# Performance work log

Hardware: AMD Instinct MI355X
Metric: run time of the kernel (lower is better)

Reference implementation:

```python
import jax, jax.numpy as jnp
import numpy as np

IN_SIZE = 1024
HID = 2048
OUT = 1024
M_STEPS = 100   # max extra ponder steps -> up to M_STEPS+1 total steps
EPS = 0.01


def setup_inputs() -> dict:
    key = jax.random.key(0)
    ks = jax.random.split(key, 11)
    inv = 1.0 / np.sqrt(HID)

    def unif(k, shape, scale):
        return jax.random.uniform(k, shape, jnp.float32, -scale, scale)

    return {
        "x": jax.random.normal(ks[0], (IN_SIZE,), jnp.float32),
        "h0": jax.random.normal(ks[1], (HID,), jnp.float32) * 0.1,
        "c0": jax.random.normal(ks[2], (HID,), jnp.float32) * 0.1,
        "W_ih": unif(ks[3], (4 * HID, 1 + IN_SIZE), inv),
        "b_ih": unif(ks[4], (4 * HID,), inv),
        "W_hh": unif(ks[5], (4 * HID, HID), inv),
        "b_hh": unif(ks[6], (4 * HID,), inv),
        "w_halt": unif(ks[7], (HID,), inv),
        "b_halt": jnp.ones((1,), jnp.float32),  # fc_halt.bias = 1.0 per source
        "W_out": unif(ks[8], (OUT, HID), inv),
        "b_out": unif(ks[9], (OUT,), inv),
    }


def reference(x, h0, c0, W_ih, b_ih, W_hh, b_hh, w_halt, b_halt, W_out, b_out):
    # Input contribution is constant across steps except the prepended halt flag
    # (1 on first step, 0 after). Precompute it once.
    ih_x = W_ih[:, 1:] @ x + b_ih + b_hh      # (4H,)
    w_flag = W_ih[:, 0]                        # (4H,)

    def step(carry, flag):
        h, c = carry
        gates = ih_x + flag * w_flag + W_hh @ h  # (4H,)
        i, f, g, o = jnp.split(gates, 4)
        i = jax.nn.sigmoid(i)
        f = jax.nn.sigmoid(f)
        g = jnp.tanh(g)
        o = jax.nn.sigmoid(o)
        c = f * c + i * g
        h = o * jnp.tanh(c)
        return (h, c), (h, c)

    flags = jnp.concatenate(
        [jnp.ones((1,), x.dtype), jnp.zeros((M_STEPS,), x.dtype)])
    _, (H, C) = jax.lax.scan(step, (h0, c0), flags)  # (M+1, HID) each

    p = jax.nn.sigmoid(H @ w_halt + b_halt[0])       # (M+1,) halting probs
    csum = jnp.cumsum(p)
    halted = csum >= 1.0 - EPS
    # n = first step where cumulative halt prob crosses threshold, capped at M
    n = jnp.where(jnp.any(halted), jnp.argmax(halted), M_STEPS)
    # remainder r = 1 - sum(p[:n]); csum[n] - p[n] == sum(p[:n])
    r = 1.0 - jnp.where(n > 0, csum[n] - p[n], 0.0)

    idx = jnp.arange(M_STEPS + 1)
    w = jnp.where(idx < n, p, jnp.where(idx == n, r, 0.0))  # (M+1,)

    outputs = H @ W_out.T + b_out                    # (M+1, OUT)
    output = w @ outputs                             # (OUT,) weights sum to 1
    h_out = w @ H                                    # (HID,)
    c_out = w @ C                                    # (HID,)
    ponder = n.astype(x.dtype) + 1.0 + r
    return output, (h_out, c_out), ponder
```

## Files before the change

### kernel.cpp

```cpp
#include <hip/hip_runtime.h>


#define HID    2048
#define INS    1024
#define OUTS   1024
#define MSTEPS 100
#define NBLK   256
#define NTHR   512
#define NWAVE  8
#define JPB    8
#define RPB    32
#define SLOTF  16

typedef unsigned long long u64;
typedef unsigned int u32;

__device__ __forceinline__ float wave_allreduce(float v) {
    #pragma unroll
    for (int off = 32; off > 0; off >>= 1)
        v += __shfl_xor(v, off, 64);
    return v;
}

__device__ __forceinline__ u64 aload(const u64* p) {
    return __hip_atomic_load(p, __ATOMIC_RELAXED, __HIP_MEMORY_SCOPE_AGENT);
}
__device__ __forceinline__ void astore(u64* p, u64 v) {
    __hip_atomic_store(p, v, __ATOMIC_RELAXED, __HIP_MEMORY_SCOPE_AGENT);
}
__device__ __forceinline__ void astoref(float* p, float v) {
    __hip_atomic_store(p, v, __ATOMIC_RELAXED, __HIP_MEMORY_SCOPE_AGENT);
}


__global__
__attribute__((amdgpu_flat_work_group_size(NTHR, NTHR)))
__attribute__((amdgpu_waves_per_eu(2, 2)))
void alstm_kernel(
    const float* __restrict__ x,      const float* __restrict__ h0,
    const float* __restrict__ c0,     const float* __restrict__ W_ih,
    const float* __restrict__ b_ih,   const float* __restrict__ W_hh,
    const float* __restrict__ b_hh,   const float* __restrict__ w_halt,
    const float* __restrict__ b_halt, const float* __restrict__ W_out,
    const float* __restrict__ b_out,  float* __restrict__ out,
    float* __restrict__ ws)
{
    const int b    = blockIdx.x;
    const int tid  = threadIdx.x;
    const int wave = tid >> 6;
    const int lane = tid & 63;

    float* arrive = ws;
    float* hbuf0  = ws + NBLK * SLOTF;
    float* hbuf1  = hbuf0 + HID;

    __shared__ float x_lds[INS];
    __shared__ float hjoint[HID];
    __shared__ float hcur[HID];
    __shared__ float gate_lds[RPB];
    __shared__ float ihx_lds[RPB];
    __shared__ float psum[NWAVE];

    const int j_own = b * JPB + tid;
    const int lr0   = 4 * wave;
    const int rbase = (lr0 >> 3) * HID + b * JPB + (lr0 & 7);

    #define DOT4(H4P, G0, G1, G2, G3) do {                                     \
        const float4* h4__ = (H4P);                                            \
        _Pragma("unroll")                                                      \
        for (int m = 0; m < 8; ++m) {                                          \
            float4 hh = h4__[lane + 64 * m];                                   \
            G0 += wa0[m].x*hh.x + wa0[m].y*hh.y + wa0[m].z*hh.z + wa0[m].w*hh.w; \
            G1 += wa1[m].x*hh.x + wa1[m].y*hh.y + wa1[m].z*hh.z + wa1[m].w*hh.w; \
            G2 += wa2[m].x*hh.x + wa2[m].y*hh.y + wa2[m].z*hh.z + wa2[m].w*hh.w; \
            G3 += wa3[m].x*hh.x + wa3[m].y*hh.y + wa3[m].z*hh.z + wa3[m].w*hh.w; \
        }                                                                      \
    } while (0)

    const float bh = b_halt[0];
    float2 xv  = ((const float2*)x)[tid];
    float4 h0v = ((const float4*)h0)[tid];
    float4 wh4 = ((const float4*)w_halt)[tid];
    float c_reg = (tid < JPB) ? c0[j_own] : 0.f;
    float bo    = (tid < 4)   ? b_out[b * 4 + tid] : 0.f;
    float bsum = 0.f, wflg = 0.f;
    if (lane < 4) {
        const int lr = lr0 + lane;
        const int r  = (lr >> 3) * HID + b * JPB + (lr & 7);
        bsum = b_ih[r] + b_hh[r];
        wflg = W_ih[(size_t)r * (INS + 1)];
    }
    __builtin_amdgcn_sched_barrier(0);

    const float*  wr_[4];
    const float4* wv_[4];
    int p0_[4];
    #pragma unroll
    for (int rr = 0; rr < 4; ++rr) {
        const int lr = lr0 + rr;
        const int r  = (lr >> 3) * HID + b * JPB + (lr & 7);
        wr_[rr] = W_ih + (size_t)r * (INS + 1) + 1;
        p0_[rr] = (4 - ((r + 1) & 3)) & 3;
        wv_[rr] = (const float4*)(wr_[rr] + p0_[rr]);
    }
    float4 iw0[4], iw1[4], iw2[4], iw3[4];
    #pragma unroll
    for (int ii = 0; ii < 4; ++ii) {
        const int i  = lane + 64 * ii;
        const int ic = (i < 255) ? i : 0;
        iw0[ii] = wv_[0][ic];
        iw1[ii] = wv_[1][ic];
        iw2[ii] = wv_[2][ic];
        iw3[ii] = wv_[3][ic];
    }
    __builtin_amdgcn_sched_barrier(0);

    float4 wa0[8], wa1[8], wa2[8], wa3[8];
    {
        const float4* s0 = (const float4*)(W_hh + (size_t)(rbase + 0) * HID);
        const float4* s1 = (const float4*)(W_hh + (size_t)(rbase + 1) * HID);
        const float4* s2 = (const float4*)(W_hh + (size_t)(rbase + 2) * HID);
        const float4* s3 = (const float4*)(W_hh + (size_t)(rbase + 3) * HID);
        #pragma unroll
        for (int m = 0; m < 8; ++m) {
            wa0[m] = s0[lane + 64 * m];
            wa1[m] = s1[lane + 64 * m];
            wa2[m] = s2[lane + 64 * m];
            wa3[m] = s3[lane + 64 * m];
        }
    }
    __builtin_amdgcn_sched_barrier(0);

    const int orow  = b * 4 + (wave & 3);
    const int ohalf = wave >> 2;
    const float4* wrow = (const float4*)(W_out + (size_t)orow * HID) + ohalf * 256;
    float4 wo0 = wrow[lane], wo1 = wrow[lane + 64],
           wo2 = wrow[lane + 128], wo3 = wrow[lane + 192];
    __builtin_amdgcn_sched_barrier(0);

    ((float2*)x_lds)[tid]  = xv;
    ((float4*)hjoint)[tid] = h0v;
    __syncthreads();

    float a0 = 0.f, a1 = 0.f, a2 = 0.f, a3 = 0.f;
    #pragma unroll
    for (int ii = 0; ii < 4; ++ii) {
        const int   i   = lane + 64 * ii;
        const int   ic  = (i < 255) ? i : 0;
        const float msk = (i < 255) ? 1.f : 0.f;
        #pragma unroll
        for (int rr = 0; rr < 4; ++rr) {
            float4 w4 = (rr == 0) ? iw0[ii] : (rr == 1) ? iw1[ii]
                      : (rr == 2) ? iw2[ii] : iw3[ii];
            const int k = p0_[rr] + 4 * ic;
            float s = w4.x * x_lds[k]     + w4.y * x_lds[k + 1]
                    + w4.z * x_lds[k + 2] + w4.w * x_lds[k + 3];
            s *= msk;
            if      (rr == 0) a0 += s;
            else if (rr == 1) a1 += s;
            else if (rr == 2) a2 += s;
            else              a3 += s;
        }
    }
    if (lane < 4) {
        #pragma unroll
        for (int rr = 0; rr < 4; ++rr) {
            const int p0 = p0_[rr];
            const int e  = (lane < p0) ? lane : 1020 + lane;
            float s = wr_[rr][e] * x_lds[e];
            if      (rr == 0) a0 += s;
            else if (rr == 1) a1 += s;
            else if (rr == 2) a2 += s;
            else              a3 += s;
        }
    }

    float g0 = 0.f, g1 = 0.f, g2 = 0.f, g3 = 0.f;
    DOT4((const float4*)hjoint, g0, g1, g2, g3);

    a0 = wave_allreduce(a0); a1 = wave_allreduce(a1);
    a2 = wave_allreduce(a2); a3 = wave_allreduce(a3);
    g0 = wave_allreduce(g0); g1 = wave_allreduce(g1);
    g2 = wave_allreduce(g2); g3 = wave_allreduce(g3);
    if (lane < 4) {
        float av = (lane == 0) ? a0 : (lane == 1) ? a1 : (lane == 2) ? a2 : a3;
        float gv = (lane == 0) ? g0 : (lane == 1) ? g1 : (lane == 2) ? g2 : g3;
        ihx_lds[lr0 + lane]  = av + bsum;
        gate_lds[lr0 + lane] = av + bsum + wflg + gv;
    }
    __syncthreads();

    float4 hb4 = make_float4(0.f, 0.f, 0.f, 0.f);
    float  h_reg = 0.f, cbar = 0.f, csum = 0.f, r_halt = 0.f;
    int    n_halt = 0;
    for (int t = 0; t <= MSTEPS; ++t) {
        float* hdst = (t & 1) ? hbuf1 : hbuf0;
        if (tid < JPB) {
            float iv = gate_lds[0 * JPB + tid];
            float fv = gate_lds[1 * JPB + tid];
            float gv = gate_lds[2 * JPB + tid];
            float ov = gate_lds[3 * JPB + tid];
            iv = 1.f / (1.f + expf(-iv));
            fv = 1.f / (1.f + expf(-fv));
            gv = tanhf(gv);
            ov = 1.f / (1.f + expf(-ov));
            c_reg = fv * c_reg + iv * gv;
            h_reg = ov * tanhf(c_reg);
            astoref(hdst + j_own, h_reg);
        }
        asm volatile("s_waitcnt vmcnt(0)" ::: "memory");
        if (tid == 0)
            astore((u64*)(arrive + SLOTF * b), (u64)(t + 1));

        if (tid < NBLK) {
            const u64* slot = (const u64*)(arrive + SLOTF * tid);
            u64 v = aload(slot);
            while (v < (u64)(t + 1)) {
                __builtin_amdgcn_s_sleep(1);
                v = aload(slot);
            }
        }
        __syncthreads();

        const u64* hsrc = (const u64*)((t & 1) ? hbuf1 : hbuf0);
        u64 hA = aload(hsrc + 2 * tid);
        u64 hB = aload(hsrc + 2 * tid + 1);
        float4 hv = make_float4(__uint_as_float((u32)hA),
                                __uint_as_float((u32)(hA >> 32)),
                                __uint_as_float((u32)hB),
                                __uint_as_float((u32)(hB >> 32)));
        ((float4*)hcur)[tid] = hv;

        float part = hv.x * wh4.x + hv.y * wh4.y + hv.z * wh4.z + hv.w * wh4.w;
        part = wave_allreduce(part);
        if (lane == 0) psum[wave] = part;
        __syncthreads();
        float dotv = ((psum[0] + psum[1]) + (psum[2] + psum[3]))
                   + ((psum[4] + psum[5]) + (psum[6] + psum[7]));
        float p = 1.f / (1.f + expf(-(dotv + bh)));
        float prev = csum;
        csum += p;
        bool  halt_now = (csum >= 1.f - 0.01f) || (t == MSTEPS);
        float wt = halt_now ? (1.f - prev) : p;
        hb4.x += wt * hv.x; hb4.y += wt * hv.y;
        hb4.z += wt * hv.z; hb4.w += wt * hv.w;
        if (tid < JPB) cbar += wt * c_reg;
        if (halt_now) { n_halt = t; r_halt = 1.f - prev; break; }

        {
            float m0 = 0.f, m1 = 0.f, m2 = 0.f, m3 = 0.f;
            DOT4((const float4*)hcur, m0, m1, m2, m3);
            m0 = wave_allreduce(m0); m1 = wave_allreduce(m1);
            m2 = wave_allreduce(m2); m3 = wave_allreduce(m3);
            if (lane < 4) {
                float mv = (lane == 0) ? m0 : (lane == 1) ? m1
                         : (lane == 2) ? m2 : m3;
                gate_lds[lr0 + lane] = ihx_lds[lr0 + lane] + mv;
            }
        }
        __syncthreads();
    }

    ((float4*)hjoint)[tid] = hb4;
    if (b == 0) ((float4*)(out + OUTS))[tid] = hb4;
    if (tid < JPB) out[OUTS + HID + j_own] = cbar;
    if (b == 0 && tid == 0) out[OUTS + 2 * HID] = (float)(n_halt + 1) + r_halt;
    __syncthreads();

    {
        const float4* hb4p = (const float4*)hjoint + ohalf * 256;
        float acc = 0.f;
        { float4 h4 = hb4p[lane];       acc += wo0.x*h4.x + wo0.y*h4.y + wo0.z*h4.z + wo0.w*h4.w; }
        { float4 h4 = hb4p[lane + 64];  acc += wo1.x*h4.x + wo1.y*h4.y + wo1.z*h4.z + wo1.w*h4.w; }
        { float4 h4 = hb4p[lane + 128]; acc += wo2.x*h4.x + wo2.y*h4.y + wo2.z*h4.z + wo2.w*h4.w; }
        { float4 h4 = hb4p[lane + 192]; acc += wo3.x*h4.x + wo3.y*h4.y + wo3.z*h4.z + wo3.w*h4.w; }
        acc = wave_allreduce(acc);
        if (lane == 0) psum[wave] = acc;
    }
    __syncthreads();
    if (tid < 4) out[b * 4 + tid] = psum[tid] + psum[tid + 4] + bo;

    #undef DOT4
}

extern "C" void kernel_launch(void* const* d_in, const int* in_sizes, int n_in,
                              void* d_out, int out_size, void* d_ws, size_t ws_size,
                              hipStream_t stream) {
    const float* x      = (const float*)d_in[0];
    const float* h0     = (const float*)d_in[1];
    const float* c0     = (const float*)d_in[2];
    const float* W_ih   = (const float*)d_in[3];
    const float* b_ih   = (const float*)d_in[4];
    const float* W_hh   = (const float*)d_in[5];
    const float* b_hh   = (const float*)d_in[6];
    const float* w_halt = (const float*)d_in[7];
    const float* b_halt = (const float*)d_in[8];
    const float* W_out  = (const float*)d_in[9];
    const float* b_out  = (const float*)d_in[10];
    float* out = (float*)d_out;
    float* ws  = (float*)d_ws;

    hipMemsetAsync(d_ws, 0, 32768, stream);

    alstm_kernel<<<dim3(NBLK), dim3(NTHR), 0, stream>>>(
        x, h0, c0, W_ih, b_ih, W_hh, b_hh, w_halt, b_halt, W_out, b_out,
        out, ws);
}
```

Before: 155.5 us.

## Double block width to 16 waves, each owning two gate rows

Raises the persistent block from 512 to 1024 threads, so each wave keeps two W_hh rows in registers instead of four and splits the W_out row into quarters. The goal is to halve the per-wave serial dot-product and reduction work on the recurrent critical path of each step. In exchange, block-wide barriers and the halting-probability reduction now span 16 waves, and occupancy settings change to 4 waves per EU, which tightens the per-thread register budget.

```diff
diff --git a/kernel.cpp b/kernel.cpp
--- a/kernel.cpp
+++ b/kernel.cpp
@@ -6,8 +6,8 @@
 #define OUTS   1024
 #define MSTEPS 100
 #define NBLK   256
-#define NTHR   512
-#define NWAVE  8
+#define NTHR   1024
+#define NWAVE  16
 #define JPB    8
 #define RPB    32
 #define SLOTF  16
@@ -35,7 +35,7 @@
 
 __global__
 __attribute__((amdgpu_flat_work_group_size(NTHR, NTHR)))
-__attribute__((amdgpu_waves_per_eu(2, 2)))
+__attribute__((amdgpu_waves_per_eu(4, 4)))
 void alstm_kernel(
     const float* __restrict__ x,      const float* __restrict__ h0,
     const float* __restrict__ c0,     const float* __restrict__ W_ih,
@@ -62,135 +62,108 @@
     __shared__ float psum[NWAVE];
 
     const int j_own = b * JPB + tid;
-    const int lr0   = 4 * wave;
-    const int rbase = (lr0 >> 3) * HID + b * JPB + (lr0 & 7);
-
-    #define DOT4(H4P, G0, G1, G2, G3) do {                                     \
+    const int lr0   = 2 * wave;
+    #define GR(lr_) (((lr_) >> 3) * HID + b * JPB + ((lr_) & 7))
+
+    #define DOT2(H4P, G0, G1) do {                                             \
         const float4* h4__ = (H4P);                                            \
         _Pragma("unroll")                                                      \
         for (int m = 0; m < 8; ++m) {                                          \
             float4 hh = h4__[lane + 64 * m];                                   \
             G0 += wa0[m].x*hh.x + wa0[m].y*hh.y + wa0[m].z*hh.z + wa0[m].w*hh.w; \
             G1 += wa1[m].x*hh.x + wa1[m].y*hh.y + wa1[m].z*hh.z + wa1[m].w*hh.w; \
-            G2 += wa2[m].x*hh.x + wa2[m].y*hh.y + wa2[m].z*hh.z + wa2[m].w*hh.w; \
-            G3 += wa3[m].x*hh.x + wa3[m].y*hh.y + wa3[m].z*hh.z + wa3[m].w*hh.w; \
         }                                                                      \
     } while (0)
 
     const float bh = b_halt[0];
-    float2 xv  = ((const float2*)x)[tid];
-    float4 h0v = ((const float4*)h0)[tid];
-    float4 wh4 = ((const float4*)w_halt)[tid];
+    float  xv  = x[tid];
+    float2 h0v = ((const float2*)h0)[tid];
+    float2 wh2 = ((const float2*)w_halt)[tid];
     float c_reg = (tid < JPB) ? c0[j_own] : 0.f;
     float bo    = (tid < 4)   ? b_out[b * 4 + tid] : 0.f;
     float bsum = 0.f, wflg = 0.f;
-    if (lane < 4) {
-        const int lr = lr0 + lane;
-        const int r  = (lr >> 3) * HID + b * JPB + (lr & 7);
+    if (lane < 2) {
+        const int r = GR(lr0 + lane);
         bsum = b_ih[r] + b_hh[r];
         wflg = W_ih[(size_t)r * (INS + 1)];
     }
     __builtin_amdgcn_sched_barrier(0);
 
-    const float*  wr_[4];
-    const float4* wv_[4];
-    int p0_[4];
-    #pragma unroll
-    for (int rr = 0; rr < 4; ++rr) {
-        const int lr = lr0 + rr;
-        const int r  = (lr >> 3) * HID + b * JPB + (lr & 7);
-        wr_[rr] = W_ih + (size_t)r * (INS + 1) + 1;
-        p0_[rr] = (4 - ((r + 1) & 3)) & 3;
-        wv_[rr] = (const float4*)(wr_[rr] + p0_[rr]);
-    }
-    float4 iw0[4], iw1[4], iw2[4], iw3[4];
+    const int rA = GR(lr0), rB = GR(lr0 + 1);
+    const float* wrA = W_ih + (size_t)rA * (INS + 1) + 1;
+    const float* wrB = W_ih + (size_t)rB * (INS + 1) + 1;
+    const int pA = (4 - ((rA + 1) & 3)) & 3;
+    const int pB = (4 - ((rB + 1) & 3)) & 3;
+    const float4* wvA = (const float4*)(wrA + pA);
+    const float4* wvB = (const float4*)(wrB + pB);
+    float4 iwA[4], iwB[4];
     #pragma unroll
     for (int ii = 0; ii < 4; ++ii) {
         const int i  = lane + 64 * ii;
         const int ic = (i < 255) ? i : 0;
-        iw0[ii] = wv_[0][ic];
-        iw1[ii] = wv_[1][ic];
-        iw2[ii] = wv_[2][ic];
-        iw3[ii] = wv_[3][ic];
+        iwA[ii] = wvA[ic];
+        iwB[ii] = wvB[ic];
     }
     __builtin_amdgcn_sched_barrier(0);
 
-    float4 wa0[8], wa1[8], wa2[8], wa3[8];
-    {
-        const float4* s0 = (const float4*)(W_hh + (size_t)(rbase + 0) * HID);
-        const float4* s1 = (const float4*)(W_hh + (size_t)(rbase + 1) * HID);
-        const float4* s2 = (const float4*)(W_hh + (size_t)(rbase + 2) * HID);
-        const float4* s3 = (const float4*)(W_hh + (size_t)(rbase + 3) * HID);
-        #pragma unroll
-        for (int m = 0; m < 8; ++m) {
-            wa0[m] = s0[lane + 64 * m];
-            wa1[m] = s1[lane + 64 * m];
-            wa2[m] = s2[lane + 64 * m];
-            wa3[m] = s3[lane + 64 * m];
-        }
-    }
-    __builtin_amdgcn_sched_barrier(0);
-
-    const int orow  = b * 4 + (wave & 3);
-    const int ohalf = wave >> 2;
-    const float4* wrow = (const float4*)(W_out + (size_t)orow * HID) + ohalf * 256;
-    float4 wo0 = wrow[lane], wo1 = wrow[lane + 64],
-           wo2 = wrow[lane + 128], wo3 = wrow[lane + 192];
-    __builtin_amdgcn_sched_barrier(0);
-
-    ((float2*)x_lds)[tid]  = xv;
-    ((float4*)hjoint)[tid] = h0v;
-    __syncthreads();
-
-    float a0 = 0.f, a1 = 0.f, a2 = 0.f, a3 = 0.f;
+    x_lds[tid] = xv;
+    ((float2*)hjoint)[tid] = h0v;
+    __syncthreads();
+
+    float a0 = 0.f, a1 = 0.f;
     #pragma unroll
     for (int ii = 0; ii < 4; ++ii) {
         const int   i   = lane + 64 * ii;
         const int   ic  = (i < 255) ? i : 0;
         const float msk = (i < 255) ? 1.f : 0.f;
+        {
+            const int k = pA + 4 * ic;
+            a0 += msk * (iwA[ii].x * x_lds[k]     + iwA[ii].y * x_lds[k + 1]
+                       + iwA[ii].z * x_lds[k + 2] + iwA[ii].w * x_lds[k + 3]);
+        }
+        {
+            const int k = pB + 4 * ic;
+            a1 += msk * (iwB[ii].x * x_lds[k]     + iwB[ii].y * x_lds[k + 1]
+                       + iwB[ii].z * x_lds[k + 2] + iwB[ii].w * x_lds[k + 3]);
+        }
+    }
+    if (lane < 4) {
+        const int eA = (lane < pA) ? lane : 1020 + lane;
+        const int eB = (lane < pB) ? lane : 1020 + lane;
+        a0 += wrA[eA] * x_lds[eA];
+        a1 += wrB[eB] * x_lds[eB];
+    }
+
+    float4 wa0[8], wa1[8];
+    {
+        const float4* s0 = (const float4*)(W_hh + (size_t)rA * HID);
+        const float4* s1 = (const float4*)(W_hh + (size_t)rB * HID);
         #pragma unroll
-        for (int rr = 0; rr < 4; ++rr) {
-            float4 w4 = (rr == 0) ? iw0[ii] : (rr == 1) ? iw1[ii]
-                      : (rr == 2) ? iw2[ii] : iw3[ii];
-            const int k = p0_[rr] + 4 * ic;
-            float s = w4.x * x_lds[k]     + w4.y * x_lds[k + 1]
-                    + w4.z * x_lds[k + 2] + w4.w * x_lds[k + 3];
-            s *= msk;
-            if      (rr == 0) a0 += s;
-            else if (rr == 1) a1 += s;
-            else if (rr == 2) a2 += s;
-            else              a3 += s;
-        }
-    }
-    if (lane < 4) {
-        #pragma unroll
-        for (int rr = 0; rr < 4; ++rr) {
-            const int p0 = p0_[rr];
-            const int e  = (lane < p0) ? lane : 1020 + lane;
-            float s = wr_[rr][e] * x_lds[e];
-            if      (rr == 0) a0 += s;
-            else if (rr == 1) a1 += s;
-            else if (rr == 2) a2 += s;
-            else              a3 += s;
-        }
-    }
-
-    float g0 = 0.f, g1 = 0.f, g2 = 0.f, g3 = 0.f;
-    DOT4((const float4*)hjoint, g0, g1, g2, g3);
+        for (int m = 0; m < 8; ++m) {
+            wa0[m] = s0[lane + 64 * m];
+            wa1[m] = s1[lane + 64 * m];
+        }
+    }
+    const int orow = b * 4 + (wave & 3);
+    const int oq   = wave >> 2;
+    const float4* wrow = (const float4*)(W_out + (size_t)orow * HID) + oq * 128;
+    float4 wo0 = wrow[lane], wo1 = wrow[lane + 64];
+    __builtin_amdgcn_sched_barrier(0);
+
+    float g0 = 0.f, g1 = 0.f;
+    DOT2((const float4*)hjoint, g0, g1);
 
     a0 = wave_allreduce(a0); a1 = wave_allreduce(a1);
-    a2 = wave_allreduce(a2); a3 = wave_allreduce(a3);
     g0 = wave_allreduce(g0); g1 = wave_allreduce(g1);
-    g2 = wave_allreduce(g2); g3 = wave_allreduce(g3);
-    if (lane < 4) {
-        float av = (lane == 0) ? a0 : (lane == 1) ? a1 : (lane == 2) ? a2 : a3;
-        float gv = (lane == 0) ? g0 : (lane == 1) ? g1 : (lane == 2) ? g2 : g3;
+    if (lane < 2) {
+        float av = lane ? a1 : a0;
+        float gv = lane ? g1 : g0;
         ihx_lds[lr0 + lane]  = av + bsum;
         gate_lds[lr0 + lane] = av + bsum + wflg + gv;
     }
     __syncthreads();
 
-    float4 hb4 = make_float4(0.f, 0.f, 0.f, 0.f);
+    float2 hb2 = make_float2(0.f, 0.f);
     float  h_reg = 0.f, cbar = 0.f, csum = 0.f, r_halt = 0.f;
     int    n_halt = 0;
     for (int t = 0; t <= MSTEPS; ++t) {
@@ -223,64 +196,60 @@
         __syncthreads();
 
         const u64* hsrc = (const u64*)((t & 1) ? hbuf1 : hbuf0);
-        u64 hA = aload(hsrc + 2 * tid);
-        u64 hB = aload(hsrc + 2 * tid + 1);
-        float4 hv = make_float4(__uint_as_float((u32)hA),
-                                __uint_as_float((u32)(hA >> 32)),
-                                __uint_as_float((u32)hB),
-                                __uint_as_float((u32)(hB >> 32)));
-        ((float4*)hcur)[tid] = hv;
-
-        float part = hv.x * wh4.x + hv.y * wh4.y + hv.z * wh4.z + hv.w * wh4.w;
+        u64 hA = aload(hsrc + tid);
+        float2 hv = make_float2(__uint_as_float((u32)hA),
+                                __uint_as_float((u32)(hA >> 32)));
+        ((float2*)hcur)[tid] = hv;
+
+        float part = hv.x * wh2.x + hv.y * wh2.y;
         part = wave_allreduce(part);
         if (lane == 0) psum[wave] = part;
         __syncthreads();
-        float dotv = ((psum[0] + psum[1]) + (psum[2] + psum[3]))
-                   + ((psum[4] + psum[5]) + (psum[6] + psum[7]));
+        float dotv = (((psum[0]  + psum[1])  + (psum[2]  + psum[3]))
+                   +  ((psum[4]  + psum[5])  + (psum[6]  + psum[7])))
+                   + (((psum[8]  + psum[9])  + (psum[10] + psum[11]))
+                   +  ((psum[12] + psum[13]) + (psum[14] + psum[15])));
         float p = 1.f / (1.f + expf(-(dotv + bh)));
         float prev = csum;
         csum += p;
         bool  halt_now = (csum >= 1.f - 0.01f) || (t == MSTEPS);
         float wt = halt_now ? (1.f - prev) : p;
-        hb4.x += wt * hv.x; hb4.y += wt * hv.y;
-        hb4.z += wt * hv.z; hb4.w += wt * hv.w;
+        hb2.x += wt * hv.x; hb2.y += wt * hv.y;
         if (tid < JPB) cbar += wt * c_reg;
         if (halt_now) { n_halt = t; r_halt = 1.f - prev; break; }
 
         {
-            float m0 = 0.f, m1 = 0.f, m2 = 0.f, m3 = 0.f;
-            DOT4((const float4*)hcur, m0, m1, m2, m3);
-            m0 = wave_allreduce(m0); m1 = wave_allreduce(m1);
-            m2 = wave_allreduce(m2); m3 = wave_allreduce(m3);
-            if (lane < 4) {
-                float mv = (lane == 0) ? m0 : (lane == 1) ? m1
-                         : (lane == 2) ? m2 : m3;
-                gate_lds[lr0 + lane] = ihx_lds[lr0 + lane] + mv;
-            }
+            float m0 = 0.f, m1 = 0.f;
+            DOT2((const float4*)hcur, m0, m1);
+            m0 = wave_allreduce(m0);
+            m1 = wave_allreduce(m1);
+            if (lane < 2)
+                gate_lds[lr0 + lane] = ihx_lds[lr0 + lane] + (lane ? m1 : m0);
         }
         __syncthreads();
     }
 
-    ((float4*)hjoint)[tid] = hb4;
-    if (b == 0) ((float4*)(out + OUTS))[tid] = hb4;
+    ((float2*)hjoint)[tid] = hb2;
+    if (b == 0) ((float2*)(out + OUTS))[tid] = hb2;
     if (tid < JPB) out[OUTS + HID + j_own] = cbar;
     if (b == 0 && tid == 0) out[OUTS + 2 * HID] = (float)(n_halt + 1) + r_halt;
     __syncthreads();
 
     {
-        const float4* hb4p = (const float4*)hjoint + ohalf * 256;
+        const float4* hb4p = (const float4*)hjoint + oq * 128;
         float acc = 0.f;
-        { float4 h4 = hb4p[lane];       acc += wo0.x*h4.x + wo0.y*h4.y + wo0.z*h4.z + wo0.w*h4.w; }
-        { float4 h4 = hb4p[lane + 64];  acc += wo1.x*h4.x + wo1.y*h4.y + wo1.z*h4.z + wo1.w*h4.w; }
-        { float4 h4 = hb4p[lane + 128]; acc += wo2.x*h4.x + wo2.y*h4.y + wo2.z*h4.z + wo2.w*h4.w; }
-        { float4 h4 = hb4p[lane + 192]; acc += wo3.x*h4.x + wo3.y*h4.y + wo3.z*h4.z + wo3.w*h4.w; }
+        { float4 h4 = hb4p[lane];      acc += wo0.x*h4.x + wo0.y*h4.y + wo0.z*h4.z + wo0.w*h4.w; }
+        { float4 h4 = hb4p[lane + 64]; acc += wo1.x*h4.x + wo1.y*h4.y + wo1.z*h4.z + wo1.w*h4.w; }
         acc = wave_allreduce(acc);
         if (lane == 0) psum[wave] = acc;
     }
     __syncthreads();
-    if (tid < 4) out[b * 4 + tid] = psum[tid] + psum[tid + 4] + bo;
-
-    #undef DOT4
+    if (tid < 4)
+        out[b * 4 + tid] = psum[tid] + psum[tid + 4] + psum[tid + 8]
+                         + psum[tid + 12] + bo;
+
+    #undef DOT2
+    #undef GR
 }
 
 extern "C" void kernel_launch(void* const* d_in, const int* in_sizes, int n_in,
```

After: 157.0 us. Within noise of the previous version (+0.9%).
